# Performance work log

Measured on AMD Instinct MI355X. Metric: run time of the kernel, lower is better.

Reference implementation:

```python
import jax, jax.numpy as jnp
import numpy as np

C = 64
K = 3  # kernel_size
B, H, W = 8, 128, 128


def conv2d(x, w, b, pad, groups=1):
    y = jax.lax.conv_general_dilated(
        x, w, window_strides=(1, 1), padding=[(pad, pad), (pad, pad)],
        feature_group_count=groups, dimension_numbers=('NCHW', 'OIHW', 'NCHW'))
    return y + b[None, :, None, None]


def setup_inputs() -> dict:
    key = jax.random.key(0)
    ks = jax.random.split(key, 11)
    s3 = 1.0 / np.sqrt(C * 9)  # kaiming-ish scale for 3x3 convs
    inp = {
        'x':  jax.random.normal(ks[0], (B, C, H, W), jnp.float32),
        'w0': jax.random.normal(ks[1], (C, C, 3, 3), jnp.float32) * s3,
        'b0': jax.random.normal(ks[2], (C,), jnp.float32) * 0.01,
        'w1': jax.random.normal(ks[3], (C, 1, 3, 3), jnp.float32) * (1.0 / 3.0),  # depthwise
        'b1': jax.random.normal(ks[4], (C,), jnp.float32) * 0.01,
        'w2': jax.random.normal(ks[5], (1, 1, K), jnp.float32) * (1.0 / np.sqrt(K)),  # conv1d over channel axis
        'b2': jax.random.normal(ks[6], (1,), jnp.float32) * 0.01,
        'w3': jax.random.normal(ks[7], (C * K * K, C, 1, 1), jnp.float32) * (1.0 / np.sqrt(C)),  # 1x1 -> dynamic filters
        'b3': jax.random.normal(ks[8], (C * K * K,), jnp.float32) * 0.01,
        'wf': jax.random.normal(ks[9], (C, C, 3, 3), jnp.float32) * s3,
        'bf': jax.random.normal(ks[10], (C,), jnp.float32) * 0.01,
    }
    return inp


def reference(x, w0, b0, w1, b1, w2, b2, w3, b3, wf, bf):
    b, c, h, w = x.shape
    pre = x
    # conv0: dense 3x3
    x0 = conv2d(x, w0, b0, pad=1)
    # conv1: depthwise 3x3
    x1 = conv2d(x0, w1, b1, pad=1, groups=c)
    # ECA-style channel attention: global avg pool -> conv1d over channel dim
    m = jnp.mean(x0, axis=(2, 3))  # [b, c]
    x2 = jax.lax.conv_general_dilated(
        m[:, None, :], w2, window_strides=(1,), padding=[(K // 2, K // 2)],
        dimension_numbers=('NCH', 'OIH', 'NCH')) + b2[None, :, None]  # [b, 1, c]
    out = x1 + x2[:, 0, :, None, None]  # broadcast [b,c,1,1] over h,w
    # conv3: 1x1 producing per-pixel dynamic filters [b, c*9, h, w]
    fil = jnp.einsum('oc,bchw->bohw', w3[:, :, 0, 0], out) + b3[None, :, None, None]
    filter_x = fil.reshape(b, c, K * K, h, w)
    # unfold(x0): 3x3 patches, channel-major then row-major kernel positions
    xp = jnp.pad(x0, ((0, 0), (0, 0), (1, 1), (1, 1)))
    unfold_x = jnp.stack(
        [xp[:, :, i:i + h, j:j + w] for i in range(3) for j in range(3)], axis=2)  # [b,c,9,h,w]
    out = jnp.sum(unfold_x * filter_x, axis=2)  # per-pixel dynamic conv
    out = jnp.where(out >= 0, out, 0.2 * out)  # LeakyReLU(0.2)
    out = conv2d(out, wf, bf, pad=1) + pre
    return out
```

## Files before the change

kernel.cpp:

```cpp
#include <hip/hip_runtime.h>

#define BB 8
#define C 64
#define HH 128
#define WW 128
#define HW (HH*WW)

#define TS 72
#define NPX 324

typedef __attribute__((ext_vector_type(8))) short short8;
typedef __attribute__((ext_vector_type(4))) float f32x4;

__device__ inline unsigned short f2bf(float f) {
    union { float f; unsigned u; } v; v.f = f;
    unsigned r = v.u + 0x7fff + ((v.u >> 16) & 1);
    return (unsigned short)(r >> 16);
}
__device__ inline float bf2f(unsigned short h) {
    union { unsigned u; float f; } v; v.u = ((unsigned)h) << 16;
    return v.f;
}

__global__ __launch_bounds__(256) void prep_kernel(
    const float* __restrict__ w0, const float* __restrict__ wf,
    const float* __restrict__ w3, const float* __restrict__ b3,
    unsigned short* __restrict__ wb0, unsigned short* __restrict__ wbf,
    unsigned short* __restrict__ wb3, float* __restrict__ b3r,
    float* __restrict__ m)
{
    const int t = blockIdx.x * 256 + threadIdx.x;
    for (int i = t; i < C*C*9; i += 32*256) {
        int p = i % 9; int rest = i / 9; int ci = rest % C; int oc = rest / C;
        wb0[(p*C + oc)*C + ci] = f2bf(w0[i]);
        wbf[(p*C + oc)*C + ci] = f2bf(wf[i]);
    }
    for (int i = t; i < 9*C*C; i += 32*256) {
        int j = i >> 12, oc = (i >> 6) & 63, k = i & 63;
        wb3[i] = f2bf(w3[(oc*9 + j)*C + k]);
    }
    for (int i = t; i < 9*C; i += 32*256) {
        int j = i >> 6, oc = i & 63;
        b3r[i] = b3[oc*9 + j];
    }
    for (int i = t; i < BB*C; i += 32*256) m[i] = 0.f;
}

template<bool FIRST>
__global__ __launch_bounds__(256) void conv_mfma_kernel(
    const void* __restrict__ in,
    const unsigned short* __restrict__ wb,
    const float* __restrict__ bias,
    const float* __restrict__ res,
    void* __restrict__ outp)
{
    __shared__ unsigned short tile[NPX*TS];
    const int b  = blockIdx.z;
    const int h0 = blockIdx.y * 16;
    const int w0 = blockIdx.x * 16;
    const int t  = threadIdx.x;

    {
        const int pxi = t & 31, g = t >> 5;
        for (int px = pxi; px < NPX; px += 32) {
            int th = px / 18, tw = px - th*18;
            int gh = h0 + th - 1, gw = w0 + tw - 1;
            short8 v = {0,0,0,0,0,0,0,0};
            if ((unsigned)gh < HH && (unsigned)gw < WW) {
                if (FIRST) {
                    const float* sp = (const float*)in
                        + ((size_t)(b*C + g*8)*HW + gh*WW + gw);
#pragma unroll
                    for (int k = 0; k < 8; ++k) v[k] = (short)f2bf(sp[k*HW]);
                } else {
                    v = *(const short8*)((const unsigned short*)in
                        + ((size_t)(b*HW) + gh*WW + gw)*C + g*8);
                }
            }
            *(short8*)&tile[px*TS + g*8] = v;
        }
    }
    __syncthreads();

    const int wid = t >> 6, ln = t & 63;
    const int l15 = ln & 15, q = ln >> 4;

    f32x4 acc[4][4];
#pragma unroll
    for (int mg = 0; mg < 4; ++mg)
#pragma unroll
        for (int nt = 0; nt < 4; ++nt) acc[mg][nt] = (f32x4){0.f,0.f,0.f,0.f};

#pragma unroll
    for (int p = 0; p < 9; ++p) {
        const int dh = p / 3, dw = p % 3;
#pragma unroll
        for (int ks = 0; ks < 2; ++ks) {
            short8 bfrag[4];
#pragma unroll
            for (int nt = 0; nt < 4; ++nt)
                bfrag[nt] = *(const short8*)&wb[((size_t)(p*C) + nt*16 + l15)*C + ks*32 + q*8];
            short8 afrag[4];
#pragma unroll
            for (int mg = 0; mg < 4; ++mg) {
                const int r = wid*4 + mg;
                afrag[mg] = *(const short8*)&tile[((r+dh)*18 + l15 + dw)*TS + ks*32 + q*8];
            }
#pragma unroll
            for (int mg = 0; mg < 4; ++mg)
#pragma unroll
                for (int nt = 0; nt < 4; ++nt)
                    acc[mg][nt] = __builtin_amdgcn_mfma_f32_16x16x32_bf16(
                        afrag[mg], bfrag[nt], acc[mg][nt], 0, 0, 0);
        }
    }

    if (FIRST) {
        unsigned short* x0 = (unsigned short*)outp;
#pragma unroll
        for (int mg = 0; mg < 4; ++mg) {
            const int hh = h0 + wid*4 + mg;
#pragma unroll
            for (int nt = 0; nt < 4; ++nt) {
                const int oc = nt*16 + l15;
                const float bv = bias[oc];
#pragma unroll
                for (int reg = 0; reg < 4; ++reg) {
                    const int wwp = w0 + q*4 + reg;
                    x0[((size_t)(b*HW) + hh*WW + wwp)*C + oc] = f2bf(acc[mg][nt][reg] + bv);
                }
            }
        }
    } else {
        float* outg = (float*)outp;
#pragma unroll
        for (int mg = 0; mg < 4; ++mg) {
            const int hh = h0 + wid*4 + mg;
#pragma unroll
            for (int nt = 0; nt < 4; ++nt) {
                const int oc = nt*16 + l15;
                const float bv = bias[oc];
                const size_t base = (size_t)(b*C + oc)*HW + hh*WW + w0 + q*4;
                const float4 rv = *(const float4*)&res[base];
                float4 ov;
                ov.x = acc[mg][nt][0] + bv + rv.x;
                ov.y = acc[mg][nt][1] + bv + rv.y;
                ov.z = acc[mg][nt][2] + bv + rv.z;
                ov.w = acc[mg][nt][3] + bv + rv.w;
                *(float4*)&outg[base] = ov;
            }
        }
    }
}

__global__ __launch_bounds__(256) void mean_kernel(
    const unsigned short* __restrict__ x0, float* __restrict__ m)
{
    const int b = blockIdx.x >> 4, slice = blockIdx.x & 15;
    const int t = threadIdx.x;
    const int pxi = t >> 3, g = t & 7;
    const unsigned short* base = x0 + ((size_t)b*HW + slice*1024)*C + g*8;
    float s[8];
#pragma unroll
    for (int k = 0; k < 8; ++k) s[k] = 0.f;
    for (int it = 0; it < 32; ++it) {
        short8 v = *(const short8*)&base[(size_t)(it*32 + pxi)*C];
#pragma unroll
        for (int k = 0; k < 8; ++k) s[k] += bf2f((unsigned short)v[k]);
    }
    __shared__ float red[32][64];
#pragma unroll
    for (int k = 0; k < 8; ++k) red[pxi][g*8+k] = s[k];
    __syncthreads();
    if (t < 64) {
        float acc = 0.f;
        for (int i = 0; i < 32; ++i) acc += red[i][t];
        atomicAdd(&m[b*C + t], acc * (1.f/(float)HW));
    }
}

__global__ __launch_bounds__(256) void fused_kernel(
    const unsigned short* __restrict__ x0,
    const float* __restrict__ w1, const float* __restrict__ b1,
    const float* __restrict__ w2, const float* __restrict__ b2,
    const unsigned short* __restrict__ wb3,
    const float* __restrict__ b3r,
    const float* __restrict__ m,
    unsigned short* __restrict__ y)
{
    __shared__ unsigned short tile[NPX*TS];
    __shared__ unsigned short alds[256*64];
    const int b  = blockIdx.z;
    const int h0 = blockIdx.y * 16;
    const int w0 = blockIdx.x * 16;
    const int t  = threadIdx.x;

    {
        const int pxi = t & 31, g = t >> 5;
        for (int px = pxi; px < NPX; px += 32) {
            int th = px / 18, tw = px - th*18;
            int gh = h0 + th - 1, gw = w0 + tw - 1;
            short8 v = {0,0,0,0,0,0,0,0};
            if ((unsigned)gh < HH && (unsigned)gw < WW)
                v = *(const short8*)&x0[((size_t)(b*HW) + gh*WW + gw)*C + g*8];
            *(short8*)&tile[px*TS + g*8] = v;
        }
    }
    __syncthreads();

    const int r = t >> 4, cc = t & 15;
    const unsigned short* tbase = tile + (r*18 + cc)*TS;

    float outv[64];
    const float w2a = w2[0], w2b = w2[1], w2c = w2[2], b2v = b2[0];
#pragma unroll
    for (int g = 0; g < 8; ++g) {
        float dw8[8];
#pragma unroll
        for (int k = 0; k < 8; ++k) dw8[k] = 0.f;
#pragma unroll
        for (int j = 0; j < 9; ++j) {
            short8 v = *(const short8*)&tbase[((j/3)*18 + (j%3))*TS + g*8];
#pragma unroll
            for (int k = 0; k < 8; ++k)
                dw8[k] = fmaf(w1[(g*8+k)*9 + j], bf2f((unsigned short)v[k]), dw8[k]);
        }
#pragma unroll
        for (int k = 0; k < 8; ++k) {
            const int c = g*8 + k;
            const float mc = m[b*C + c];
            const float mp = (c > 0)  ? m[b*C + c - 1] : 0.f;
            const float mn = (c < 63) ? m[b*C + c + 1] : 0.f;
            outv[c] = dw8[k] + b1[c] + fmaf(w2a, mp, fmaf(w2b, mc, fmaf(w2c, mn, b2v)));
        }
    }

    {
        const int sw = t & 7;
#pragma unroll
        for (int g = 0; g < 8; ++g) {
            short8 v;
#pragma unroll
            for (int k = 0; k < 8; ++k) v[k] = (short)f2bf(outv[g*8 + k]);
            *(short8*)&alds[t*64 + ((g ^ sw) * 8)] = v;
        }
    }
    __syncthreads();

    const int wid = t >> 6, ln = t & 63;
    const int l15 = ln & 15, q = ln >> 4;

    short8 afrag[4][2];
#pragma unroll
    for (int mg = 0; mg < 4; ++mg) {
        const int px = (wid*4 + mg)*16 + l15;
        const int sw = px & 7;
#pragma unroll
        for (int ks = 0; ks < 2; ++ks)
            afrag[mg][ks] = *(const short8*)&alds[px*64 + (((ks*4 + q) ^ sw) * 8)];
    }

    f32x4 y_acc[4][4];
#pragma unroll
    for (int mg = 0; mg < 4; ++mg)
#pragma unroll
        for (int nt = 0; nt < 4; ++nt) y_acc[mg][nt] = (f32x4){0.f,0.f,0.f,0.f};

#pragma unroll
    for (int j = 0; j < 9; ++j) {
        const int dh = j / 3, dw = j % 3;
#pragma unroll
        for (int ntoc = 0; ntoc < 4; ++ntoc) {
            const int oc = ntoc*16 + l15;
            const float b3v = b3r[j*64 + oc];
            const short8 bf0 = *(const short8*)&wb3[((size_t)(j*64 + oc))*64 + q*8];
            const short8 bf1 = *(const short8*)&wb3[((size_t)(j*64 + oc))*64 + 32 + q*8];
            f32x4 fil[4];
#pragma unroll
            for (int mg = 0; mg < 4; ++mg) {
                f32x4 a = (f32x4){b3v, b3v, b3v, b3v};
                a = __builtin_amdgcn_mfma_f32_16x16x32_bf16(afrag[mg][0], bf0, a, 0, 0, 0);
                a = __builtin_amdgcn_mfma_f32_16x16x32_bf16(afrag[mg][1], bf1, a, 0, 0, 0);
                fil[mg] = a;
            }
#pragma unroll
            for (int mg = 0; mg < 4; ++mg) {
                const int rr = wid*4 + mg;
                const unsigned short* pb = &tile[((rr+dh)*18 + q*4 + dw)*TS + oc];
#pragma unroll
                for (int reg = 0; reg < 4; ++reg) {
                    const float pv = bf2f(pb[reg*TS]);
                    y_acc[mg][ntoc][reg] = fmaf(fil[mg][reg], pv, y_acc[mg][ntoc][reg]);
                }
            }
        }
    }

    __syncthreads();
    unsigned short* ybuf = alds;
#pragma unroll
    for (int mg = 0; mg < 4; ++mg) {
        const int rr = wid*4 + mg;
#pragma unroll
        for (int ntoc = 0; ntoc < 4; ++ntoc) {
            const int oc = ntoc*16 + l15;
#pragma unroll
            for (int reg = 0; reg < 4; ++reg) {
                float v = y_acc[mg][ntoc][reg];
                v = (v >= 0.f) ? v : 0.2f * v;
                ybuf[(rr*16 + q*4 + reg)*64 + oc] = f2bf(v);
            }
        }
    }
    __syncthreads();
    for (int id = t; id < 2048; id += 256) {
        int px = id >> 3, g = id & 7;
        short8 v = *(const short8*)&ybuf[px*64 + g*8];
        int rr = px >> 4, cw = px & 15;
        *(short8*)&y[((size_t)(b*HW) + (h0+rr)*WW + (w0+cw))*C + g*8] = v;
    }
}

extern "C" void kernel_launch(void* const* d_in, const int* in_sizes, int n_in,
                              void* d_out, int out_size, void* d_ws, size_t ws_size,
                              hipStream_t stream) {
    const float* x  = (const float*)d_in[0];
    const float* w0 = (const float*)d_in[1];
    const float* b0 = (const float*)d_in[2];
    const float* w1 = (const float*)d_in[3];
    const float* b1 = (const float*)d_in[4];
    const float* w2 = (const float*)d_in[5];
    const float* b2 = (const float*)d_in[6];
    const float* w3 = (const float*)d_in[7];
    const float* b3 = (const float*)d_in[8];
    const float* wf = (const float*)d_in[9];
    const float* bf = (const float*)d_in[10];
    float* out = (float*)d_out;

    unsigned short* x0  = (unsigned short*)d_ws;
    unsigned short* y   = x0 + (size_t)BB*HW*C;
    float*          m   = (float*)(y + (size_t)BB*HW*C);
    unsigned short* wb0 = (unsigned short*)(m + BB*C);
    unsigned short* wbf = wb0 + 9*C*C;
    unsigned short* wb3 = wbf + 9*C*C;
    float*          b3r = (float*)(wb3 + 9*C*C);

    prep_kernel<<<32, 256, 0, stream>>>(w0, wf, w3, b3, wb0, wbf, wb3, b3r, m);
    conv_mfma_kernel<true><<<dim3(8,8,8), 256, 0, stream>>>(x, wb0, b0, nullptr, x0);
    mean_kernel<<<128, 256, 0, stream>>>(x0, m);
    fused_kernel<<<dim3(8,8,8), 256, 0, stream>>>(x0, w1, b1, w2, b2, wb3, b3r, m, y);
    conv_mfma_kernel<false><<<dim3(8,8,8), 256, 0, stream>>>(y, wbf, bf, x, out);
}
```

Measured before the change: 223.6 us.

## Split fused depthwise/dynamic-conv kernel and transpose MFMA operands for vector stores

The fused depthwise+ECA+dynamic-filter kernel becomes two kernels: a per-pixel depthwise/ECA kernel that writes an intermediate bf16 tensor to global memory, and a dynamic-conv kernel that reads it directly as MFMA fragments. This drops the large LDS staging buffer and its syncs, which should raise occupancy. conv0 swaps the A/B MFMA operands so each lane holds four consecutive output channels, allowing packed 8-byte channel-last stores instead of scalar 2-byte ones. Launch-bounds occupancy hints are added. The cost is an extra kernel launch and an extra full-size intermediate written and read through global memory.

New measurement: 363.1 us. 62.4% more time.

```diff
diff --git a/kernel.cpp b/kernel.cpp
--- a/kernel.cpp
+++ b/kernel.cpp
@@ -10,6 +10,7 @@
 #define NPX 324
 
 typedef __attribute__((ext_vector_type(8))) short short8;
+typedef __attribute__((ext_vector_type(4))) short short4v;
 typedef __attribute__((ext_vector_type(4))) float f32x4;
 
 __device__ inline unsigned short f2bf(float f) {
@@ -46,13 +47,11 @@
     for (int i = t; i < BB*C; i += 32*256) m[i] = 0.f;
 }
 
-template<bool FIRST>
-__global__ __launch_bounds__(256) void conv_mfma_kernel(
-    const void* __restrict__ in,
+__global__ __launch_bounds__(256, 3) void conv0_kernel(
+    const float* __restrict__ x,
     const unsigned short* __restrict__ wb,
     const float* __restrict__ bias,
-    const float* __restrict__ res,
-    void* __restrict__ outp)
+    unsigned short* __restrict__ x0g)
 {
     __shared__ unsigned short tile[NPX*TS];
     const int b  = blockIdx.z;
@@ -67,15 +66,9 @@
             int gh = h0 + th - 1, gw = w0 + tw - 1;
             short8 v = {0,0,0,0,0,0,0,0};
             if ((unsigned)gh < HH && (unsigned)gw < WW) {
-                if (FIRST) {
-                    const float* sp = (const float*)in
-                        + ((size_t)(b*C + g*8)*HW + gh*WW + gw);
-#pragma unroll
-                    for (int k = 0; k < 8; ++k) v[k] = (short)f2bf(sp[k*HW]);
-                } else {
-                    v = *(const short8*)((const unsigned short*)in
-                        + ((size_t)(b*HW) + gh*WW + gw)*C + g*8);
-                }
+                const float* sp = x + ((size_t)(b*C + g*8)*HW + gh*WW + gw);
+#pragma unroll
+                for (int k = 0; k < 8; ++k) v[k] = (short)f2bf(sp[k*HW]);
             }
             *(short8*)&tile[px*TS + g*8] = v;
         }
@@ -87,68 +80,46 @@
 
     f32x4 acc[4][4];
 #pragma unroll
-    for (int mg = 0; mg < 4; ++mg)
-#pragma unroll
-        for (int nt = 0; nt < 4; ++nt) acc[mg][nt] = (f32x4){0.f,0.f,0.f,0.f};
+    for (int nt = 0; nt < 4; ++nt)
+#pragma unroll
+        for (int mt = 0; mt < 4; ++mt) acc[nt][mt] = (f32x4){0.f,0.f,0.f,0.f};
 
 #pragma unroll
     for (int p = 0; p < 9; ++p) {
         const int dh = p / 3, dw = p % 3;
 #pragma unroll
         for (int ks = 0; ks < 2; ++ks) {
-            short8 bfrag[4];
+            short8 af[4];
+#pragma unroll
+            for (int mt = 0; mt < 4; ++mt)
+                af[mt] = *(const short8*)&wb[((size_t)(p*C) + mt*16 + l15)*C + ks*32 + q*8];
+            short8 bf[4];
 #pragma unroll
             for (int nt = 0; nt < 4; ++nt)
-                bfrag[nt] = *(const short8*)&wb[((size_t)(p*C) + nt*16 + l15)*C + ks*32 + q*8];
-            short8 afrag[4];
-#pragma unroll
-            for (int mg = 0; mg < 4; ++mg) {
-                const int r = wid*4 + mg;
-                afrag[mg] = *(const short8*)&tile[((r+dh)*18 + l15 + dw)*TS + ks*32 + q*8];
-            }
-#pragma unroll
-            for (int mg = 0; mg < 4; ++mg)
-#pragma unroll
-                for (int nt = 0; nt < 4; ++nt)
-                    acc[mg][nt] = __builtin_amdgcn_mfma_f32_16x16x32_bf16(
-                        afrag[mg], bfrag[nt], acc[mg][nt], 0, 0, 0);
-        }
-    }
-
-    if (FIRST) {
-        unsigned short* x0 = (unsigned short*)outp;
-#pragma unroll
-        for (int mg = 0; mg < 4; ++mg) {
-            const int hh = h0 + wid*4 + mg;
-#pragma unroll
-            for (int nt = 0; nt < 4; ++nt) {
-                const int oc = nt*16 + l15;
-                const float bv = bias[oc];
-#pragma unroll
-                for (int reg = 0; reg < 4; ++reg) {
-                    const int wwp = w0 + q*4 + reg;
-                    x0[((size_t)(b*HW) + hh*WW + wwp)*C + oc] = f2bf(acc[mg][nt][reg] + bv);
-                }
-            }
-        }
-    } else {
-        float* outg = (float*)outp;
-#pragma unroll
-        for (int mg = 0; mg < 4; ++mg) {
-            const int hh = h0 + wid*4 + mg;
-#pragma unroll
-            for (int nt = 0; nt < 4; ++nt) {
-                const int oc = nt*16 + l15;
-                const float bv = bias[oc];
-                const size_t base = (size_t)(b*C + oc)*HW + hh*WW + w0 + q*4;
-                const float4 rv = *(const float4*)&res[base];
-                float4 ov;
-                ov.x = acc[mg][nt][0] + bv + rv.x;
-                ov.y = acc[mg][nt][1] + bv + rv.y;
-                ov.z = acc[mg][nt][2] + bv + rv.z;
-                ov.w = acc[mg][nt][3] + bv + rv.w;
-                *(float4*)&outg[base] = ov;
-            }
+                bf[nt] = *(const short8*)&tile[((wid*4+nt+dh)*18 + l15 + dw)*TS + ks*32 + q*8];
+#pragma unroll
+            for (int nt = 0; nt < 4; ++nt)
+#pragma unroll
+                for (int mt = 0; mt < 4; ++mt)
+                    acc[nt][mt] = __builtin_amdgcn_mfma_f32_16x16x32_bf16(
+                        af[mt], bf[nt], acc[nt][mt], 0, 0, 0);
+        }
+    }
+
+#pragma unroll
+    for (int nt = 0; nt < 4; ++nt) {
+        const int hh = h0 + wid*4 + nt;
+        const size_t base = ((size_t)(b*HW) + hh*WW + w0 + l15)*C;
+#pragma unroll
+        for (int mt = 0; mt < 4; ++mt) {
+            const int oc0 = mt*16 + q*4;
+            const float4 bv = *(const float4*)&bias[oc0];
+            unsigned u0 = (unsigned)f2bf(acc[nt][mt][0] + bv.x)
+                        | ((unsigned)f2bf(acc[nt][mt][1] + bv.y) << 16);
+            unsigned u1 = (unsigned)f2bf(acc[nt][mt][2] + bv.z)
+                        | ((unsigned)f2bf(acc[nt][mt][3] + bv.w) << 16);
+            uint2 uu; uu.x = u0; uu.y = u1;
+            *(uint2*)&x0g[base + oc0] = uu;
         }
     }
 }
@@ -179,17 +150,56 @@
     }
 }
 
-__global__ __launch_bounds__(256) void fused_kernel(
+__global__ __launch_bounds__(256, 4) void dw_eca_kernel(
     const unsigned short* __restrict__ x0,
     const float* __restrict__ w1, const float* __restrict__ b1,
     const float* __restrict__ w2, const float* __restrict__ b2,
+    const float* __restrict__ m,
+    unsigned short* __restrict__ aout)
+{
+    const int tg = blockIdx.x * 256 + threadIdx.x;
+    const int b = tg >> 14, px = tg & 16383;
+    const int h = px >> 7, w = px & 127;
+    const unsigned short* xb = x0 + (size_t)(b*HW)*C;
+    const float w2a = w2[0], w2b = w2[1], w2c = w2[2], b2v = b2[0];
+
+#pragma unroll
+    for (int g = 0; g < 8; ++g) {
+        float dw8[8];
+#pragma unroll
+        for (int k = 0; k < 8; ++k) dw8[k] = 0.f;
+#pragma unroll
+        for (int j = 0; j < 9; ++j) {
+            const int nh = h + j/3 - 1, nw = w + j%3 - 1;
+            short8 v = {0,0,0,0,0,0,0,0};
+            if ((unsigned)nh < HH && (unsigned)nw < WW)
+                v = *(const short8*)&xb[(size_t)(nh*WW + nw)*C + g*8];
+#pragma unroll
+            for (int k = 0; k < 8; ++k)
+                dw8[k] = fmaf(w1[(g*8+k)*9 + j], bf2f((unsigned short)v[k]), dw8[k]);
+        }
+        short8 o;
+#pragma unroll
+        for (int k = 0; k < 8; ++k) {
+            const int c = g*8 + k;
+            const float mc = m[b*C + c];
+            const float mp = (c > 0)  ? m[b*C + c - 1] : 0.f;
+            const float mn = (c < 63) ? m[b*C + c + 1] : 0.f;
+            const float att = fmaf(w2a, mp, fmaf(w2b, mc, fmaf(w2c, mn, b2v)));
+            o[k] = (short)f2bf(dw8[k] + b1[c] + att);
+        }
+        *(short8*)&aout[(size_t)(b*HW + px)*C + g*8] = o;
+    }
+}
+
+__global__ __launch_bounds__(256, 3) void dynconv_kernel(
+    const unsigned short* __restrict__ x0,
+    const unsigned short* __restrict__ aout,
     const unsigned short* __restrict__ wb3,
     const float* __restrict__ b3r,
-    const float* __restrict__ m,
-    unsigned short* __restrict__ y)
+    unsigned short* __restrict__ yg)
 {
     __shared__ unsigned short tile[NPX*TS];
-    __shared__ unsigned short alds[256*64];
     const int b  = blockIdx.z;
     const int h0 = blockIdx.y * 16;
     const int w0 = blockIdx.x * 16;
@@ -208,116 +218,141 @@
     }
     __syncthreads();
 
-    const int r = t >> 4, cc = t & 15;
-    const unsigned short* tbase = tile + (r*18 + cc)*TS;
-
-    float outv[64];
-    const float w2a = w2[0], w2b = w2[1], w2c = w2[2], b2v = b2[0];
-#pragma unroll
-    for (int g = 0; g < 8; ++g) {
-        float dw8[8];
-#pragma unroll
-        for (int k = 0; k < 8; ++k) dw8[k] = 0.f;
-#pragma unroll
-        for (int j = 0; j < 9; ++j) {
-            short8 v = *(const short8*)&tbase[((j/3)*18 + (j%3))*TS + g*8];
-#pragma unroll
-            for (int k = 0; k < 8; ++k)
-                dw8[k] = fmaf(w1[(g*8+k)*9 + j], bf2f((unsigned short)v[k]), dw8[k]);
-        }
-#pragma unroll
-        for (int k = 0; k < 8; ++k) {
-            const int c = g*8 + k;
-            const float mc = m[b*C + c];
-            const float mp = (c > 0)  ? m[b*C + c - 1] : 0.f;
-            const float mn = (c < 63) ? m[b*C + c + 1] : 0.f;
-            outv[c] = dw8[k] + b1[c] + fmaf(w2a, mp, fmaf(w2b, mc, fmaf(w2c, mn, b2v)));
-        }
-    }
-
-    {
-        const int sw = t & 7;
-#pragma unroll
-        for (int g = 0; g < 8; ++g) {
-            short8 v;
-#pragma unroll
-            for (int k = 0; k < 8; ++k) v[k] = (short)f2bf(outv[g*8 + k]);
-            *(short8*)&alds[t*64 + ((g ^ sw) * 8)] = v;
-        }
-    }
-    __syncthreads();
-
     const int wid = t >> 6, ln = t & 63;
     const int l15 = ln & 15, q = ln >> 4;
-
-    short8 afrag[4][2];
-#pragma unroll
-    for (int mg = 0; mg < 4; ++mg) {
-        const int px = (wid*4 + mg)*16 + l15;
-        const int sw = px & 7;
+    const int rl0 = wid*4;
+
+    short8 pfrag[4][2];
+#pragma unroll
+    for (int nt = 0; nt < 4; ++nt) {
+        const size_t pbase = ((size_t)(b*HW) + (h0+rl0+nt)*WW + w0 + l15)*C;
 #pragma unroll
         for (int ks = 0; ks < 2; ++ks)
-            afrag[mg][ks] = *(const short8*)&alds[px*64 + (((ks*4 + q) ^ sw) * 8)];
-    }
-
-    f32x4 y_acc[4][4];
-#pragma unroll
-    for (int mg = 0; mg < 4; ++mg)
-#pragma unroll
-        for (int nt = 0; nt < 4; ++nt) y_acc[mg][nt] = (f32x4){0.f,0.f,0.f,0.f};
-
-#pragma unroll
-    for (int j = 0; j < 9; ++j) {
-        const int dh = j / 3, dw = j % 3;
-#pragma unroll
-        for (int ntoc = 0; ntoc < 4; ++ntoc) {
-            const int oc = ntoc*16 + l15;
-            const float b3v = b3r[j*64 + oc];
-            const short8 bf0 = *(const short8*)&wb3[((size_t)(j*64 + oc))*64 + q*8];
-            const short8 bf1 = *(const short8*)&wb3[((size_t)(j*64 + oc))*64 + 32 + q*8];
-            f32x4 fil[4];
-#pragma unroll
-            for (int mg = 0; mg < 4; ++mg) {
-                f32x4 a = (f32x4){b3v, b3v, b3v, b3v};
-                a = __builtin_amdgcn_mfma_f32_16x16x32_bf16(afrag[mg][0], bf0, a, 0, 0, 0);
-                a = __builtin_amdgcn_mfma_f32_16x16x32_bf16(afrag[mg][1], bf1, a, 0, 0, 0);
-                fil[mg] = a;
-            }
-#pragma unroll
-            for (int mg = 0; mg < 4; ++mg) {
-                const int rr = wid*4 + mg;
-                const unsigned short* pb = &tile[((rr+dh)*18 + q*4 + dw)*TS + oc];
-#pragma unroll
-                for (int reg = 0; reg < 4; ++reg) {
-                    const float pv = bf2f(pb[reg*TS]);
-                    y_acc[mg][ntoc][reg] = fmaf(fil[mg][reg], pv, y_acc[mg][ntoc][reg]);
+            pfrag[nt][ks] = *(const short8*)&aout[pbase + ks*32 + q*8];
+    }
+
+    f32x4 yac[4][4];
+#pragma unroll
+    for (int nt = 0; nt < 4; ++nt)
+#pragma unroll
+        for (int og = 0; og < 4; ++og) yac[nt][og] = (f32x4){0.f,0.f,0.f,0.f};
+
+    for (int dh = 0; dh < 3; ++dh) {
+        for (int dw = 0; dw < 3; ++dw) {
+            const int j = dh*3 + dw;
+#pragma unroll
+            for (int og = 0; og < 4; ++og) {
+                const f32x4 seed = *(const f32x4*)&b3r[j*64 + og*16 + q*4];
+                const size_t abase = ((size_t)(j*64 + og*16 + l15))*C;
+                const short8 a0 = *(const short8*)&wb3[abase + q*8];
+                const short8 a1 = *(const short8*)&wb3[abase + 32 + q*8];
+#pragma unroll
+                for (int nt = 0; nt < 4; ++nt) {
+                    f32x4 fil = __builtin_amdgcn_mfma_f32_16x16x32_bf16(
+                        a0, pfrag[nt][0], seed, 0, 0, 0);
+                    fil = __builtin_amdgcn_mfma_f32_16x16x32_bf16(
+                        a1, pfrag[nt][1], fil, 0, 0, 0);
+                    const short4v pv = *(const short4v*)
+                        &tile[((rl0+nt+dh)*18 + l15 + dw)*TS + og*16 + q*4];
+#pragma unroll
+                    for (int reg = 0; reg < 4; ++reg)
+                        yac[nt][og][reg] = fmaf(fil[reg],
+                            bf2f((unsigned short)pv[reg]), yac[nt][og][reg]);
                 }
             }
         }
     }
 
+#pragma unroll
+    for (int nt = 0; nt < 4; ++nt) {
+        const size_t base = ((size_t)(b*HW) + (h0+rl0+nt)*WW + w0 + l15)*C;
+#pragma unroll
+        for (int og = 0; og < 4; ++og) {
+            f32x4 v = yac[nt][og];
+#pragma unroll
+            for (int reg = 0; reg < 4; ++reg)
+                v[reg] = (v[reg] >= 0.f) ? v[reg] : 0.2f * v[reg];
+            unsigned u0 = (unsigned)f2bf(v[0]) | ((unsigned)f2bf(v[1]) << 16);
+            unsigned u1 = (unsigned)f2bf(v[2]) | ((unsigned)f2bf(v[3]) << 16);
+            uint2 uu; uu.x = u0; uu.y = u1;
+            *(uint2*)&yg[base + og*16 + q*4] = uu;
+        }
+    }
+}
+
+__global__ __launch_bounds__(256, 3) void convf_kernel(
+    const unsigned short* __restrict__ yg,
+    const unsigned short* __restrict__ wb,
+    const float* __restrict__ bias,
+    const float* __restrict__ res,
+    float* __restrict__ outg)
+{
+    __shared__ unsigned short tile[NPX*TS];
+    const int b  = blockIdx.z;
+    const int h0 = blockIdx.y * 16;
+    const int w0 = blockIdx.x * 16;
+    const int t  = threadIdx.x;
+
+    {
+        const int pxi = t & 31, g = t >> 5;
+        for (int px = pxi; px < NPX; px += 32) {
+            int th = px / 18, tw = px - th*18;
+            int gh = h0 + th - 1, gw = w0 + tw - 1;
+            short8 v = {0,0,0,0,0,0,0,0};
+            if ((unsigned)gh < HH && (unsigned)gw < WW)
+                v = *(const short8*)&yg[((size_t)(b*HW) + gh*WW + gw)*C + g*8];
+            *(short8*)&tile[px*TS + g*8] = v;
+        }
+    }
     __syncthreads();
-    unsigned short* ybuf = alds;
+
+    const int wid = t >> 6, ln = t & 63;
+    const int l15 = ln & 15, q = ln >> 4;
+
+    f32x4 acc[4][4];
+#pragma unroll
+    for (int mg = 0; mg < 4; ++mg)
+#pragma unroll
+        for (int nt = 0; nt < 4; ++nt) acc[mg][nt] = (f32x4){0.f,0.f,0.f,0.f};
+
+#pragma unroll
+    for (int p = 0; p < 9; ++p) {
+        const int dh = p / 3, dw = p % 3;
+#pragma unroll
+        for (int ks = 0; ks < 2; ++ks) {
+            short8 bfrag[4];
+#pragma unroll
+            for (int nt = 0; nt < 4; ++nt)
+                bfrag[nt] = *(const short8*)&wb[((size_t)(p*C) + nt*16 + l15)*C + ks*32 + q*8];
+            short8 afrag[4];
+#pragma unroll
+            for (int mg = 0; mg < 4; ++mg)
+                afrag[mg] = *(const short8*)&tile[((wid*4+mg+dh)*18 + l15 + dw)*TS + ks*32 + q*8];
+#pragma unroll
+            for (int mg = 0; mg < 4; ++mg)
+#pragma unroll
+                for (int nt = 0; nt < 4; ++nt)
+                    acc[mg][nt] = __builtin_amdgcn_mfma_f32_16x16x32_bf16(
+                        afrag[mg], bfrag[nt], acc[mg][nt], 0, 0, 0);
+        }
+    }
+
 #pragma unroll
     for (int mg = 0; mg < 4; ++mg) {
-        const int rr = wid*4 + mg;
-#pragma unroll
-        for (int ntoc = 0; ntoc < 4; ++ntoc) {
-            const int oc = ntoc*16 + l15;
-#pragma unroll
-            for (int reg = 0; reg < 4; ++reg) {
-                float v = y_acc[mg][ntoc][reg];
-                v = (v >= 0.f) ? v : 0.2f * v;
-                ybuf[(rr*16 + q*4 + reg)*64 + oc] = f2bf(v);
-            }
-        }
-    }
-    __syncthreads();
-    for (int id = t; id < 2048; id += 256) {
-        int px = id >> 3, g = id & 7;
-        short8 v = *(const short8*)&ybuf[px*64 + g*8];
-        int rr = px >> 4, cw = px & 15;
-        *(short8*)&y[((size_t)(b*HW) + (h0+rr)*WW + (w0+cw))*C + g*8] = v;
+        const int hh = h0 + wid*4 + mg;
+#pragma unroll
+        for (int nt = 0; nt < 4; ++nt) {
+            const int oc = nt*16 + l15;
+            const float bv = bias[oc];
+            const size_t base = (size_t)(b*C + oc)*HW + hh*WW + w0 + q*4;
+            const float4 rv = *(const float4*)&res[base];
+            float4 ov;
+            ov.x = acc[mg][nt][0] + bv + rv.x;
+            ov.y = acc[mg][nt][1] + bv + rv.y;
+            ov.z = acc[mg][nt][2] + bv + rv.z;
+            ov.w = acc[mg][nt][3] + bv + rv.w;
+            *(float4*)&outg[base] = ov;
+        }
     }
 }
 
@@ -338,16 +373,18 @@
     float* out = (float*)d_out;
 
     unsigned short* x0  = (unsigned short*)d_ws;
-    unsigned short* y   = x0 + (size_t)BB*HW*C;
-    float*          m   = (float*)(y + (size_t)BB*HW*C);
+    unsigned short* y   = x0  + (size_t)BB*HW*C;
+    unsigned short* ao  = y   + (size_t)BB*HW*C;
+    float*          m   = (float*)(ao + (size_t)BB*HW*C);
     unsigned short* wb0 = (unsigned short*)(m + BB*C);
     unsigned short* wbf = wb0 + 9*C*C;
     unsigned short* wb3 = wbf + 9*C*C;
     float*          b3r = (float*)(wb3 + 9*C*C);
 
     prep_kernel<<<32, 256, 0, stream>>>(w0, wf, w3, b3, wb0, wbf, wb3, b3r, m);
-    conv_mfma_kernel<true><<<dim3(8,8,8), 256, 0, stream>>>(x, wb0, b0, nullptr, x0);
+    conv0_kernel<<<dim3(8,8,8), 256, 0, stream>>>(x, wb0, b0, x0);
     mean_kernel<<<128, 256, 0, stream>>>(x0, m);
-    fused_kernel<<<dim3(8,8,8), 256, 0, stream>>>(x0, w1, b1, w2, b2, wb3, b3r, m, y);
-    conv_mfma_kernel<false><<<dim3(8,8,8), 256, 0, stream>>>(y, wbf, bf, x, out);
-}
+    dw_eca_kernel<<<512, 256, 0, stream>>>(x0, w1, b1, w2, b2, m, ao);
+    dynconv_kernel<<<dim3(8,8,8), 256, 0, stream>>>(x0, ao, wb3, b3r, y);
+    convf_kernel<<<dim3(8,8,8), 256, 0, stream>>>(y, wbf, bf, x, out);
+}
```
